# Kernel tuning notes

Measured on AMD Instinct MI355X. Metric: run time of the kernel, lower is better.

The kernel has to match this reference:

```python
import jax, jax.numpy as jnp
import numpy as np

D = 512
B, N = 8, 2048

def setup_inputs() -> dict:
    key = jax.random.key(0)
    ks = jax.random.split(key, 11)
    s = 1.0 / np.sqrt(D)
    return {
        "X": jax.random.normal(ks[0], (B, N, D), dtype=jnp.float32),
        "intensity": jax.random.uniform(ks[1], (B, N, N), dtype=jnp.float32),
        "WQ_w": jax.random.normal(ks[2], (D, D), dtype=jnp.float32) * s,
        "WQ_b": jax.random.normal(ks[3], (D,), dtype=jnp.float32) * 0.01,
        "WK_w": jax.random.normal(ks[4], (D, D), dtype=jnp.float32) * s,
        "WK_b": jax.random.normal(ks[5], (D,), dtype=jnp.float32) * 0.01,
        "WV_w": jax.random.normal(ks[6], (D, D), dtype=jnp.float32) * s,
        "WV_b": jax.random.normal(ks[7], (D,), dtype=jnp.float32) * 0.01,
        "out_w": jax.random.normal(ks[8], (D, D), dtype=jnp.float32) * s,
        "out_b": jax.random.normal(ks[9], (D,), dtype=jnp.float32) * 0.01,
    }

def reference(X, intensity, WQ_w, WQ_b, WK_w, WK_b, WV_w, WV_b, out_w, out_b):
    # torch Linear: y = x @ W.T + b  (W is [out, in])
    q = jnp.einsum('bnd,ed->bne', X, WQ_w) + WQ_b          # [B,N,D]
    k = jnp.einsum('bnd,ed->bne', X, WK_w) + WK_b          # [B,N,D]
    v = jnp.einsum('bnd,ed->bne', X, WV_w) + WV_b          # [B,N,D]
    scale = 1.0 / np.sqrt(D).astype(np.float32)
    scores = jnp.einsum('bqd,bkd->bqk', q, k) * scale      # [B,N,N]
    attn = jax.nn.softmax(scores, axis=-1) + intensity     # post-softmax additive bias
    out = jnp.einsum('bqk,bkd->bqd', attn, v)              # [B,N,D]
    return jnp.einsum('bnd,ed->bne', out, out_w) + out_b
```

## Files before the change

kernel.cpp:

```cpp
#include <hip/hip_runtime.h>
#include <stdint.h>

typedef unsigned short ushort_t;
typedef __attribute__((__ext_vector_type__(8))) __bf16 bf16x8;
typedef __attribute__((__ext_vector_type__(4))) float f32x4;

__device__ inline ushort_t f2bf(float f) {
    unsigned int u = __float_as_uint(f);
    u = u + 0x7FFFu + ((u >> 16) & 1u);
    return (ushort_t)(u >> 16);
}
__device__ inline float bf2f(ushort_t h) {
    return __uint_as_float(((unsigned int)h) << 16);
}

#define GLOAD16(gp, lp) __builtin_amdgcn_global_load_lds( \
    (__attribute__((address_space(1))) void*)(gp),        \
    (__attribute__((address_space(3))) void*)(lp), 16, 0, 0)

template<int MODE, int BN, int BK>
__global__ __launch_bounds__(256)
void gemm_nt(const ushort_t* __restrict__ A, const ushort_t* __restrict__ B,
             void* __restrict__ Cv, const float* __restrict__ bias,
             int K, int lda, int ldb, int ldc, float scale,
             long long sA, long long sB, long long sC)
{
    constexpr int WN  = BN / 2;
    constexpr int NR  = WN / 16;
    constexpr int GPR = BK / 8;
    constexpr int AG  = 128 * GPR;
    constexpr int BG  = BN * GPR;
    __shared__ __align__(16) char lds[(128 + BN) * BK * 2];
    char* ldsA = lds;
    char* ldsB = lds + 128 * BK * 2;

    const int t = threadIdx.x;

    const int gx = gridDim.x, gy = gridDim.y;
    const int nwg = gx * gy * gridDim.z;
    int h = (blockIdx.z * gy + blockIdx.y) * gx + blockIdx.x;
    int logical = (h & 7) * (nwg >> 3) + (h >> 3);
    const int bx = logical % gx;
    const int tmp = logical / gx;
    const int by = tmp % gy;
    const int z  = tmp / gy;

    A += (size_t)z * (size_t)sA;
    B += (size_t)z * (size_t)sB;

    const int rowBase = by * 128;
    const int colBase = bx * BN;

    const int w    = t >> 6;
    const int lane = t & 63;
    const int wr = w >> 1, wc = w & 1;
    const int lr = lane & 15, lg = lane >> 4;

    f32x4 acc[4][NR];
#pragma unroll
    for (int i = 0; i < 4; ++i)
#pragma unroll
        for (int j = 0; j < NR; ++j)
            acc[i][j] = (f32x4){0.f, 0.f, 0.f, 0.f};

    for (int kt = 0; kt < K; kt += BK) {
#pragma unroll
        for (int i = 0; i < AG / 256; ++i) {
            const int L = i * 256 + t;
            const int row = L / GPR, g = L % GPR;
            GLOAD16(A + (size_t)(rowBase + row) * (size_t)lda + (kt + g * 8),
                    ldsA + L * 16);
        }
#pragma unroll
        for (int i = 0; i < BG / 256; ++i) {
            const int L = i * 256 + t;
            const int row = L / GPR, g = L % GPR;
            GLOAD16(B + (size_t)(colBase + row) * (size_t)ldb + (kt + g * 8),
                    ldsB + L * 16);
        }
        __syncthreads();

        const bf16x8* A8 = (const bf16x8*)ldsA;
        const bf16x8* B8 = (const bf16x8*)ldsB;
#pragma unroll
        for (int kk = 0; kk < BK / 32; ++kk) {
            bf16x8 af[4], bq[NR];
#pragma unroll
            for (int mi = 0; mi < 4; ++mi)
                af[mi] = A8[(wr * 64 + mi * 16 + lr) * GPR + kk * 4 + lg];
#pragma unroll
            for (int ni = 0; ni < NR; ++ni)
                bq[ni] = B8[(wc * WN + ni * 16 + lr) * GPR + kk * 4 + lg];
#pragma unroll
            for (int mi = 0; mi < 4; ++mi)
#pragma unroll
                for (int ni = 0; ni < NR; ++ni)
                    acc[mi][ni] = __builtin_amdgcn_mfma_f32_16x16x32_bf16(
                        af[mi], bq[ni], acc[mi][ni], 0, 0, 0);
        }
        __syncthreads();
    }

#pragma unroll
    for (int mi = 0; mi < 4; ++mi) {
#pragma unroll
        for (int ni = 0; ni < NR; ++ni) {
#pragma unroll
            for (int r = 0; r < 4; ++r) {
                const int grow = rowBase + wr * 64 + mi * 16 + lg * 4 + r;
                const int gcol = colBase + wc * WN + ni * 16 + lr;
                float v = acc[mi][ni][r] * scale;
                if (MODE == 0) {
                    if (bias) v += bias[gcol];
                    ushort_t* C = (ushort_t*)Cv + (size_t)z * (size_t)sC;
                    C[(size_t)grow * (size_t)ldc + gcol] = f2bf(v);
                } else if (MODE == 3) {
                    float* C = (float*)Cv;
                    C[(size_t)grow * (size_t)ldc + gcol] = v + bias[gcol];
                } else if (MODE == 4) {
                    v += bias[gcol];
                    const int seg = gcol >> 9, c = gcol & 511;
                    ushort_t* C = (ushort_t*)Cv;
                    C[(size_t)seg * 8388608 + (size_t)grow * 512 + c] = f2bf(v);
                } else {
                    ushort_t* C = (ushort_t*)Cv + (size_t)z * (size_t)sC;
                    C[(size_t)grow * (size_t)ldc + gcol] = f2bf(__expf(v));
                }
            }
        }
    }
}

__global__ __launch_bounds__(256)
void transpose_v(const ushort_t* __restrict__ V, ushort_t* __restrict__ Vt)
{
    __shared__ ushort_t lds[64][68];
    const int t = threadIdx.x;
    const int nBase = blockIdx.x * 64;
    const int dBase = blockIdx.y * 64;
    const size_t b = blockIdx.z;
    const ushort_t* src = V + b * 1048576;
    ushort_t* dst = Vt + b * 1048576;
#pragma unroll
    for (int i = 0; i < 2; ++i) {
        int s = i * 256 + t;
        int n = s >> 3, dg = s & 7;
        union { ushort_t h[8]; uint4 u; } p;
        p.u = *(const uint4*)(src + (size_t)(nBase + n) * 512 + dBase + dg * 8);
#pragma unroll
        for (int j = 0; j < 8; ++j) lds[n][dg * 8 + j] = p.h[j];
    }
    __syncthreads();
#pragma unroll
    for (int i = 0; i < 2; ++i) {
        int s = i * 256 + t;
        int d = s >> 3, ng = s & 7;
        union { ushort_t h[8]; uint4 u; } p;
#pragma unroll
        for (int j = 0; j < 8; ++j) p.h[j] = lds[ng * 8 + j][d];
        *(uint4*)(dst + (size_t)(dBase + d) * 2048 + nBase + ng * 8) = p.u;
    }
}

__global__ __launch_bounds__(256)
void cvt_bf16(const float* __restrict__ src, ushort_t* __restrict__ dst, int n4)
{
    int i = blockIdx.x * 256 + threadIdx.x;
    if (i >= n4) return;
    float4 v = ((const float4*)src)[i];
    union { ushort_t h[4]; uint2 u; } p;
    p.h[0] = f2bf(v.x); p.h[1] = f2bf(v.y); p.h[2] = f2bf(v.z); p.h[3] = f2bf(v.w);
    ((uint2*)dst)[i] = p.u;
}

__global__ __launch_bounds__(256)
void pack_bias(const float* __restrict__ q, const float* __restrict__ k,
               const float* __restrict__ v, float* __restrict__ dst)
{
    int i = blockIdx.x * 256 + threadIdx.x;
    if (i < 512) dst[i] = q[i];
    else if (i < 1024) dst[i] = k[i - 512];
    else if (i < 1536) dst[i] = v[i - 1024];
}

__global__ __launch_bounds__(256)
void norm_add(ushort_t* __restrict__ E, const float* __restrict__ inten)
{
    const int R = blockIdx.x;
    const int t = threadIdx.x;
    const int w = t >> 6, lane = t & 63;
    ushort_t* erow = E + (size_t)R * 2048;
    const float* irow = inten + (size_t)R * 2048;

    union { ushort_t h[8]; uint4 u; } p;
    p.u = *(const uint4*)(erow + t * 8);
    float f[8];
#pragma unroll
    for (int j = 0; j < 8; ++j) f[j] = bf2f(p.h[j]);

    float s = 0.f;
#pragma unroll
    for (int j = 0; j < 8; ++j) s += f[j];
#pragma unroll
    for (int off = 32; off > 0; off >>= 1) s += __shfl_xor(s, off);

    __shared__ float red[4];
    if (lane == 0) red[w] = s;
    __syncthreads();
    const float inv = 1.f / (red[0] + red[1] + red[2] + red[3]);

    float4 i0 = *(const float4*)(irow + t * 8);
    float4 i1 = *(const float4*)(irow + t * 8 + 4);
    float o[8] = { f[0]*inv + i0.x, f[1]*inv + i0.y, f[2]*inv + i0.z, f[3]*inv + i0.w,
                   f[4]*inv + i1.x, f[5]*inv + i1.y, f[6]*inv + i1.z, f[7]*inv + i1.w };
#pragma unroll
    for (int j = 0; j < 8; ++j) p.h[j] = f2bf(o[j]);
    *(uint4*)(erow + t * 8) = p.u;
}

extern "C" void kernel_launch(void* const* d_in, const int* in_sizes, int n_in,
                              void* d_out, int out_size, void* d_ws, size_t ws_size,
                              hipStream_t stream)
{
    const float* X    = (const float*)d_in[0];
    const float* inten= (const float*)d_in[1];
    const float* WQw  = (const float*)d_in[2];
    const float* WQb  = (const float*)d_in[3];
    const float* WKw  = (const float*)d_in[4];
    const float* WKb  = (const float*)d_in[5];
    const float* WVw  = (const float*)d_in[6];
    const float* WVb  = (const float*)d_in[7];
    const float* Wow  = (const float*)d_in[8];
    const float* Wob  = (const float*)d_in[9];
    float* out = (float*)d_out;

    char* ws = (char*)d_ws;
    ushort_t* Xb    = (ushort_t*)(ws + 0);
    ushort_t* Wqkv  = (ushort_t*)(ws + 16777216);
    ushort_t* Wob2  = (ushort_t*)(ws + 18350080);
    float*    biasP = (float*)   (ws + 18874368);
    ushort_t* QKV   = (ushort_t*)(ws + 19922944);
    ushort_t* out1  = (ushort_t*)(ws + 70254592);
    ushort_t* Sbf   = (ushort_t*)(ws + 87031808);
    ushort_t* Qb = QKV;
    ushort_t* Kb = QKV + 8388608;
    ushort_t* Vrm = QKV + 16777216;
    ushort_t* Vt  = Xb;

    const float scale = 0.044194173824159216f;

    cvt_bf16<<<dim3(8192), dim3(256), 0, stream>>>(X,   Xb, 2097152);
    cvt_bf16<<<dim3(256),  dim3(256), 0, stream>>>(WQw, Wqkv,           65536);
    cvt_bf16<<<dim3(256),  dim3(256), 0, stream>>>(WKw, Wqkv + 262144,  65536);
    cvt_bf16<<<dim3(256),  dim3(256), 0, stream>>>(WVw, Wqkv + 524288,  65536);
    cvt_bf16<<<dim3(256),  dim3(256), 0, stream>>>(Wow, Wob2,           65536);
    pack_bias<<<dim3(6),  dim3(256), 0, stream>>>(WQb, WKb, WVb, biasP);

    gemm_nt<4, 128, 32><<<dim3(12, 128, 1), dim3(256), 0, stream>>>(
        Xb, Wqkv, QKV, biasP, 512, 512, 512, 0, 1.f, 0, 0, 0);

    transpose_v<<<dim3(32, 8, 8), dim3(256), 0, stream>>>(Vrm, Vt);

    gemm_nt<5, 128, 32><<<dim3(16, 16, 8), dim3(256), 0, stream>>>(
        Qb, Kb, Sbf, nullptr, 512, 512, 512, 2048, scale,
        2048LL * 512, 2048LL * 512, 2048LL * 2048);

    norm_add<<<dim3(16384), dim3(256), 0, stream>>>(Sbf, inten);

    gemm_nt<0, 64, 32><<<dim3(8, 16, 8), dim3(256), 0, stream>>>(
        Sbf, Vt, out1, nullptr, 2048, 2048, 2048, 512, 1.f,
        2048LL * 2048, 512LL * 2048, 2048LL * 512);

    gemm_nt<3, 64, 32><<<dim3(8, 128, 1), dim3(256), 0, stream>>>(
        out1, Wob2, out, Wob, 512, 512, 512, 512, 1.f, 0, 0, 0);
}
```

Measured before the change: 243.3 us.

## Fuse softmax normalization and intensity add into PV GEMM A-tile load

Removes the separate norm_add pass. The score GEMM epilogue now accumulates per-row exp sums with atomics, a tiny kernel turns them into reciprocals, and the PV GEMM builds each A tile in registers from exp scores, the reciprocal and the fp32 intensity. The standalone X-to-bf16 conversion is also folded into the QKV projection's A load through register staging. The cost is that intensity is now read by every column block of the PV GEMM, leaning on cache for reuse. The A operand also moves from async global-to-LDS loads to register-staged loads with only one-tile prefetch.

```diff
diff --git a/kernel.cpp b/kernel.cpp
--- a/kernel.cpp
+++ b/kernel.cpp
@@ -13,17 +13,22 @@
 __device__ inline float bf2f(ushort_t h) {
     return __uint_as_float(((unsigned int)h) << 16);
 }
+__device__ inline unsigned pack2(float a, float b) {
+    return (unsigned)f2bf(a) | ((unsigned)f2bf(b) << 16);
+}
 
 #define GLOAD16(gp, lp) __builtin_amdgcn_global_load_lds( \
     (__attribute__((address_space(1))) void*)(gp),        \
     (__attribute__((address_space(3))) void*)(lp), 16, 0, 0)
 
-template<int MODE, int BN, int BK>
-__global__ __launch_bounds__(256)
-void gemm_nt(const ushort_t* __restrict__ A, const ushort_t* __restrict__ B,
+template<int MODE, int BN, int BK, int STG>
+__global__ __launch_bounds__(256)
+void gemm_nt(const void* __restrict__ Av, const ushort_t* __restrict__ B,
              void* __restrict__ Cv, const float* __restrict__ bias,
+             const float* __restrict__ If, const float* __restrict__ invp,
              int K, int lda, int ldb, int ldc, float scale,
-             long long sA, long long sB, long long sC)
+             long long sA, long long sB, long long sC,
+             float* __restrict__ rsum)
 {
     constexpr int WN  = BN / 2;
     constexpr int NR  = WN / 16;
@@ -45,7 +50,10 @@
     const int by = tmp % gy;
     const int z  = tmp / gy;
 
-    A += (size_t)z * (size_t)sA;
+    const ushort_t* A = (const ushort_t*)Av + (size_t)z * (size_t)sA;
+    const float* Af   = (const float*)Av + (size_t)z * (size_t)sA;
+    const float* Iz   = If ? If + (size_t)z * (size_t)sA : nullptr;
+    const float* invz = invp ? invp + (size_t)z * 2048 : nullptr;
     B += (size_t)z * (size_t)sB;
 
     const int rowBase = by * 128;
@@ -63,13 +71,67 @@
         for (int j = 0; j < NR; ++j)
             acc[i][j] = (f32x4){0.f, 0.f, 0.f, 0.f};
 
+    float4 xR[4];
+    uint4  eR[2]; float4 iA[2], iB[2];
+    float  invR[2];
+
+    auto loadA = [&](int kt) {
+        if constexpr (STG == 1) {
+#pragma unroll
+            for (int i = 0; i < 2; ++i) {
+                const int L = i * 256 + t, row = L >> 2, g = L & 3;
+                const float* xp = Af + (size_t)(rowBase + row) * (size_t)lda + kt + g * 8;
+                xR[2 * i]     = *(const float4*)xp;
+                xR[2 * i + 1] = *(const float4*)(xp + 4);
+            }
+        } else if constexpr (STG == 2) {
+#pragma unroll
+            for (int i = 0; i < 2; ++i) {
+                const int L = i * 256 + t, row = L >> 2, g = L & 3;
+                const ushort_t* ep = A + (size_t)(rowBase + row) * (size_t)lda + kt + g * 8;
+                eR[i] = *(const uint4*)ep;
+                const float* ip = Iz + (size_t)(rowBase + row) * (size_t)lda + kt + g * 8;
+                iA[i] = *(const float4*)ip;
+                iB[i] = *(const float4*)(ip + 4);
+                invR[i] = invz[rowBase + row];
+            }
+        }
+    };
+    auto storeA = [&]() {
+#pragma unroll
+        for (int i = 0; i < 2; ++i) {
+            const int L = i * 256 + t;
+            uint4 o;
+            if constexpr (STG == 1) {
+                o.x = pack2(xR[2*i].x, xR[2*i].y);
+                o.y = pack2(xR[2*i].z, xR[2*i].w);
+                o.z = pack2(xR[2*i+1].x, xR[2*i+1].y);
+                o.w = pack2(xR[2*i+1].z, xR[2*i+1].w);
+            } else {
+                union { ushort_t hh[8]; uint4 u; } e; e.u = eR[i];
+                const float iv = invR[i];
+                o.x = pack2(bf2f(e.hh[0]) * iv + iA[i].x, bf2f(e.hh[1]) * iv + iA[i].y);
+                o.y = pack2(bf2f(e.hh[2]) * iv + iA[i].z, bf2f(e.hh[3]) * iv + iA[i].w);
+                o.z = pack2(bf2f(e.hh[4]) * iv + iB[i].x, bf2f(e.hh[5]) * iv + iB[i].y);
+                o.w = pack2(bf2f(e.hh[6]) * iv + iB[i].z, bf2f(e.hh[7]) * iv + iB[i].w);
+            }
+            *(uint4*)(ldsA + (size_t)L * 16) = o;
+        }
+    };
+
+    if constexpr (STG != 0) loadA(0);
+
     for (int kt = 0; kt < K; kt += BK) {
-#pragma unroll
-        for (int i = 0; i < AG / 256; ++i) {
-            const int L = i * 256 + t;
-            const int row = L / GPR, g = L % GPR;
-            GLOAD16(A + (size_t)(rowBase + row) * (size_t)lda + (kt + g * 8),
-                    ldsA + L * 16);
+        if constexpr (STG == 0) {
+#pragma unroll
+            for (int i = 0; i < AG / 256; ++i) {
+                const int L = i * 256 + t;
+                const int row = L / GPR, g = L % GPR;
+                GLOAD16(A + (size_t)(rowBase + row) * (size_t)lda + (kt + g * 8),
+                        ldsA + L * 16);
+            }
+        } else {
+            storeA();
         }
 #pragma unroll
         for (int i = 0; i < BG / 256; ++i) {
@@ -78,6 +140,7 @@
             GLOAD16(B + (size_t)(colBase + row) * (size_t)ldb + (kt + g * 8),
                     ldsB + L * 16);
         }
+        if constexpr (STG != 0) { if (kt + BK < K) loadA(kt + BK); }
         __syncthreads();
 
         const bf16x8* A8 = (const bf16x8*)ldsA;
@@ -99,6 +162,14 @@
                         af[mi], bq[ni], acc[mi][ni], 0, 0, 0);
         }
         __syncthreads();
+    }
+
+    float rs[4][4];
+    if (MODE == 5) {
+#pragma unroll
+        for (int mi = 0; mi < 4; ++mi)
+#pragma unroll
+            for (int r = 0; r < 4; ++r) rs[mi][r] = 0.f;
     }
 
 #pragma unroll
@@ -123,8 +194,28 @@
                     ushort_t* C = (ushort_t*)Cv;
                     C[(size_t)seg * 8388608 + (size_t)grow * 512 + c] = f2bf(v);
                 } else {
+                    float e = __expf(v);
                     ushort_t* C = (ushort_t*)Cv + (size_t)z * (size_t)sC;
-                    C[(size_t)grow * (size_t)ldc + gcol] = f2bf(__expf(v));
+                    C[(size_t)grow * (size_t)ldc + gcol] = f2bf(e);
+                    rs[mi][r] += e;
+                }
+            }
+        }
+    }
+
+    if (MODE == 5) {
+#pragma unroll
+        for (int mi = 0; mi < 4; ++mi) {
+#pragma unroll
+            for (int r = 0; r < 4; ++r) {
+                float s = rs[mi][r];
+                s += __shfl_xor(s, 1);
+                s += __shfl_xor(s, 2);
+                s += __shfl_xor(s, 4);
+                s += __shfl_xor(s, 8);
+                if (lr == 0) {
+                    const int grow = rowBase + wr * 64 + mi * 16 + lg * 4 + r;
+                    atomicAdd(&rsum[z * 2048 + grow], s);
                 }
             }
         }
@@ -184,38 +275,17 @@
 }
 
 __global__ __launch_bounds__(256)
-void norm_add(ushort_t* __restrict__ E, const float* __restrict__ inten)
-{
-    const int R = blockIdx.x;
-    const int t = threadIdx.x;
-    const int w = t >> 6, lane = t & 63;
-    ushort_t* erow = E + (size_t)R * 2048;
-    const float* irow = inten + (size_t)R * 2048;
-
-    union { ushort_t h[8]; uint4 u; } p;
-    p.u = *(const uint4*)(erow + t * 8);
-    float f[8];
-#pragma unroll
-    for (int j = 0; j < 8; ++j) f[j] = bf2f(p.h[j]);
-
-    float s = 0.f;
-#pragma unroll
-    for (int j = 0; j < 8; ++j) s += f[j];
-#pragma unroll
-    for (int off = 32; off > 0; off >>= 1) s += __shfl_xor(s, off);
-
-    __shared__ float red[4];
-    if (lane == 0) red[w] = s;
-    __syncthreads();
-    const float inv = 1.f / (red[0] + red[1] + red[2] + red[3]);
-
-    float4 i0 = *(const float4*)(irow + t * 8);
-    float4 i1 = *(const float4*)(irow + t * 8 + 4);
-    float o[8] = { f[0]*inv + i0.x, f[1]*inv + i0.y, f[2]*inv + i0.z, f[3]*inv + i0.w,
-                   f[4]*inv + i1.x, f[5]*inv + i1.y, f[6]*inv + i1.z, f[7]*inv + i1.w };
-#pragma unroll
-    for (int j = 0; j < 8; ++j) p.h[j] = f2bf(o[j]);
-    *(uint4*)(erow + t * 8) = p.u;
+void zero_f32(float* __restrict__ p, int n)
+{
+    int i = blockIdx.x * 256 + threadIdx.x;
+    if (i < n) p[i] = 0.f;
+}
+
+__global__ __launch_bounds__(256)
+void recip_f32(float* __restrict__ p, int n)
+{
+    int i = blockIdx.x * 256 + threadIdx.x;
+    if (i < n) p[i] = 1.0f / p[i];
 }
 
 extern "C" void kernel_launch(void* const* d_in, const int* in_sizes, int n_in,
@@ -235,42 +305,46 @@
     float* out = (float*)d_out;
 
     char* ws = (char*)d_ws;
-    ushort_t* Xb    = (ushort_t*)(ws + 0);
+    ushort_t* Vt    = (ushort_t*)(ws + 0);
     ushort_t* Wqkv  = (ushort_t*)(ws + 16777216);
     ushort_t* Wob2  = (ushort_t*)(ws + 18350080);
     float*    biasP = (float*)   (ws + 18874368);
+    float*    rowsum= (float*)   (ws + 18882560);
     ushort_t* QKV   = (ushort_t*)(ws + 19922944);
     ushort_t* out1  = (ushort_t*)(ws + 70254592);
     ushort_t* Sbf   = (ushort_t*)(ws + 87031808);
-    ushort_t* Qb = QKV;
-    ushort_t* Kb = QKV + 8388608;
+    ushort_t* Qb  = QKV;
+    ushort_t* Kb  = QKV + 8388608;
     ushort_t* Vrm = QKV + 16777216;
-    ushort_t* Vt  = Xb;
 
     const float scale = 0.044194173824159216f;
 
-    cvt_bf16<<<dim3(8192), dim3(256), 0, stream>>>(X,   Xb, 2097152);
-    cvt_bf16<<<dim3(256),  dim3(256), 0, stream>>>(WQw, Wqkv,           65536);
-    cvt_bf16<<<dim3(256),  dim3(256), 0, stream>>>(WKw, Wqkv + 262144,  65536);
-    cvt_bf16<<<dim3(256),  dim3(256), 0, stream>>>(WVw, Wqkv + 524288,  65536);
-    cvt_bf16<<<dim3(256),  dim3(256), 0, stream>>>(Wow, Wob2,           65536);
-    pack_bias<<<dim3(6),  dim3(256), 0, stream>>>(WQb, WKb, WVb, biasP);
-
-    gemm_nt<4, 128, 32><<<dim3(12, 128, 1), dim3(256), 0, stream>>>(
-        Xb, Wqkv, QKV, biasP, 512, 512, 512, 0, 1.f, 0, 0, 0);
+    cvt_bf16<<<dim3(256), dim3(256), 0, stream>>>(WQw, Wqkv,          65536);
+    cvt_bf16<<<dim3(256), dim3(256), 0, stream>>>(WKw, Wqkv + 262144, 65536);
+    cvt_bf16<<<dim3(256), dim3(256), 0, stream>>>(WVw, Wqkv + 524288, 65536);
+    cvt_bf16<<<dim3(256), dim3(256), 0, stream>>>(Wow, Wob2,          65536);
+    pack_bias<<<dim3(6), dim3(256), 0, stream>>>(WQb, WKb, WVb, biasP);
+    zero_f32<<<dim3(64), dim3(256), 0, stream>>>(rowsum, 16384);
+
+    gemm_nt<4, 128, 32, 1><<<dim3(12, 128, 1), dim3(256), 0, stream>>>(
+        X, Wqkv, QKV, biasP, nullptr, nullptr,
+        512, 512, 512, 0, 1.f, 0, 0, 0, nullptr);
 
     transpose_v<<<dim3(32, 8, 8), dim3(256), 0, stream>>>(Vrm, Vt);
 
-    gemm_nt<5, 128, 32><<<dim3(16, 16, 8), dim3(256), 0, stream>>>(
-        Qb, Kb, Sbf, nullptr, 512, 512, 512, 2048, scale,
-        2048LL * 512, 2048LL * 512, 2048LL * 2048);
-
-    norm_add<<<dim3(16384), dim3(256), 0, stream>>>(Sbf, inten);
-
-    gemm_nt<0, 64, 32><<<dim3(8, 16, 8), dim3(256), 0, stream>>>(
-        Sbf, Vt, out1, nullptr, 2048, 2048, 2048, 512, 1.f,
-        2048LL * 2048, 512LL * 2048, 2048LL * 512);
-
-    gemm_nt<3, 64, 32><<<dim3(8, 128, 1), dim3(256), 0, stream>>>(
-        out1, Wob2, out, Wob, 512, 512, 512, 512, 1.f, 0, 0, 0);
-}
+    gemm_nt<5, 128, 32, 0><<<dim3(16, 16, 8), dim3(256), 0, stream>>>(
+        Qb, Kb, Sbf, nullptr, nullptr, nullptr,
+        512, 512, 512, 2048, scale,
+        2048LL * 512, 2048LL * 512, 2048LL * 2048, rowsum);
+
+    recip_f32<<<dim3(64), dim3(256), 0, stream>>>(rowsum, 16384);
+
+    gemm_nt<0, 64, 32, 2><<<dim3(8, 16, 8), dim3(256), 0, stream>>>(
+        Sbf, Vt, out1, nullptr, inten, rowsum,
+        2048, 2048, 2048, 512, 1.f,
+        2048LL * 2048, 512LL * 2048, 2048LL * 512, nullptr);
+
+    gemm_nt<3, 64, 32, 0><<<dim3(8, 128, 1), dim3(256), 0, stream>>>(
+        out1, Wob2, out, Wob, nullptr, nullptr,
+        512, 512, 512, 512, 1.f, 0, 0, 0, nullptr);
+}
```

Result: slower. 319.6 us (+31.4%).

## Fuse softmax row-sum into score GEMM epilogue via atomics; flatten normalize kernel

Applied to the files above, without the earlier changes.

The score GEMM epilogue now accumulates per-row sums of exp values, reduces them across lanes with shuffles, and atomically adds them to a row-sum buffer that is zeroed beforehand. The per-row norm_add kernel, which reread each row to compute its sum, is replaced by a grid-stride elementwise kernel that scales by the precomputed inverse sum and adds intensity. This removes the in-kernel reduction and block sync. The cost is float atomics, an extra zeroing launch, and row sums taken in fp32 before bf16 rounding. The bf16 copy of X also moves to its own workspace region instead of sharing space with the transposed V.

```diff
diff --git a/kernel.cpp b/kernel.cpp
--- a/kernel.cpp
+++ b/kernel.cpp
@@ -23,7 +23,8 @@
 void gemm_nt(const ushort_t* __restrict__ A, const ushort_t* __restrict__ B,
              void* __restrict__ Cv, const float* __restrict__ bias,
              int K, int lda, int ldb, int ldc, float scale,
-             long long sA, long long sB, long long sC)
+             long long sA, long long sB, long long sC,
+             float* __restrict__ rsum)
 {
     constexpr int WN  = BN / 2;
     constexpr int NR  = WN / 16;
@@ -99,6 +100,14 @@
                         af[mi], bq[ni], acc[mi][ni], 0, 0, 0);
         }
         __syncthreads();
+    }
+
+    float rs[4][4];
+    if (MODE == 5) {
+#pragma unroll
+        for (int mi = 0; mi < 4; ++mi)
+#pragma unroll
+            for (int r = 0; r < 4; ++r) rs[mi][r] = 0.f;
     }
 
 #pragma unroll
@@ -123,8 +132,28 @@
                     ushort_t* C = (ushort_t*)Cv;
                     C[(size_t)seg * 8388608 + (size_t)grow * 512 + c] = f2bf(v);
                 } else {
+                    float e = __expf(v);
                     ushort_t* C = (ushort_t*)Cv + (size_t)z * (size_t)sC;
-                    C[(size_t)grow * (size_t)ldc + gcol] = f2bf(__expf(v));
+                    C[(size_t)grow * (size_t)ldc + gcol] = f2bf(e);
+                    rs[mi][r] += e;
+                }
+            }
+        }
+    }
+
+    if (MODE == 5) {
+#pragma unroll
+        for (int mi = 0; mi < 4; ++mi) {
+#pragma unroll
+            for (int r = 0; r < 4; ++r) {
+                float s = rs[mi][r];
+                s += __shfl_xor(s, 1);
+                s += __shfl_xor(s, 2);
+                s += __shfl_xor(s, 4);
+                s += __shfl_xor(s, 8);
+                if (lr == 0) {
+                    const int grow = rowBase + wr * 64 + mi * 16 + lg * 4 + r;
+                    atomicAdd(&rsum[z * 2048 + grow], s);
                 }
             }
         }
@@ -184,38 +213,34 @@
 }
 
 __global__ __launch_bounds__(256)
-void norm_add(ushort_t* __restrict__ E, const float* __restrict__ inten)
-{
-    const int R = blockIdx.x;
-    const int t = threadIdx.x;
-    const int w = t >> 6, lane = t & 63;
-    ushort_t* erow = E + (size_t)R * 2048;
-    const float* irow = inten + (size_t)R * 2048;
-
-    union { ushort_t h[8]; uint4 u; } p;
-    p.u = *(const uint4*)(erow + t * 8);
-    float f[8];
-#pragma unroll
-    for (int j = 0; j < 8; ++j) f[j] = bf2f(p.h[j]);
-
-    float s = 0.f;
-#pragma unroll
-    for (int j = 0; j < 8; ++j) s += f[j];
-#pragma unroll
-    for (int off = 32; off > 0; off >>= 1) s += __shfl_xor(s, off);
-
-    __shared__ float red[4];
-    if (lane == 0) red[w] = s;
-    __syncthreads();
-    const float inv = 1.f / (red[0] + red[1] + red[2] + red[3]);
-
-    float4 i0 = *(const float4*)(irow + t * 8);
-    float4 i1 = *(const float4*)(irow + t * 8 + 4);
-    float o[8] = { f[0]*inv + i0.x, f[1]*inv + i0.y, f[2]*inv + i0.z, f[3]*inv + i0.w,
-                   f[4]*inv + i1.x, f[5]*inv + i1.y, f[6]*inv + i1.z, f[7]*inv + i1.w };
-#pragma unroll
-    for (int j = 0; j < 8; ++j) p.h[j] = f2bf(o[j]);
-    *(uint4*)(erow + t * 8) = p.u;
+void zero_f32(float* __restrict__ p, int n)
+{
+    int i = blockIdx.x * 256 + threadIdx.x;
+    if (i < n) p[i] = 0.f;
+}
+
+__global__ __launch_bounds__(256)
+void norm_flat(ushort_t* __restrict__ E, const float* __restrict__ rowsum,
+               const float* __restrict__ inten)
+{
+    const int nG = 4194304;
+    for (int g = blockIdx.x * 256 + threadIdx.x; g < nG; g += gridDim.x * 256) {
+        const size_t e0 = (size_t)g * 8;
+        const float iv = 1.0f / rowsum[e0 >> 11];
+        union { ushort_t h[8]; uint4 u; } p;
+        p.u = *(const uint4*)(E + e0);
+        float4 i0 = *(const float4*)(inten + e0);
+        float4 i1 = *(const float4*)(inten + e0 + 4);
+        p.h[0] = f2bf(bf2f(p.h[0]) * iv + i0.x);
+        p.h[1] = f2bf(bf2f(p.h[1]) * iv + i0.y);
+        p.h[2] = f2bf(bf2f(p.h[2]) * iv + i0.z);
+        p.h[3] = f2bf(bf2f(p.h[3]) * iv + i0.w);
+        p.h[4] = f2bf(bf2f(p.h[4]) * iv + i1.x);
+        p.h[5] = f2bf(bf2f(p.h[5]) * iv + i1.y);
+        p.h[6] = f2bf(bf2f(p.h[6]) * iv + i1.z);
+        p.h[7] = f2bf(bf2f(p.h[7]) * iv + i1.w);
+        *(uint4*)(E + e0) = p.u;
+    }
 }
 
 extern "C" void kernel_launch(void* const* d_in, const int* in_sizes, int n_in,
@@ -235,42 +260,44 @@
     float* out = (float*)d_out;
 
     char* ws = (char*)d_ws;
-    ushort_t* Xb    = (ushort_t*)(ws + 0);
+    ushort_t* Vt    = (ushort_t*)(ws + 0);
     ushort_t* Wqkv  = (ushort_t*)(ws + 16777216);
     ushort_t* Wob2  = (ushort_t*)(ws + 18350080);
     float*    biasP = (float*)   (ws + 18874368);
+    float*    rowsum= (float*)   (ws + 18882560);
     ushort_t* QKV   = (ushort_t*)(ws + 19922944);
     ushort_t* out1  = (ushort_t*)(ws + 70254592);
     ushort_t* Sbf   = (ushort_t*)(ws + 87031808);
-    ushort_t* Qb = QKV;
-    ushort_t* Kb = QKV + 8388608;
+    ushort_t* Xb    = (ushort_t*)(ws + 154140672);
+    ushort_t* Qb  = QKV;
+    ushort_t* Kb  = QKV + 8388608;
     ushort_t* Vrm = QKV + 16777216;
-    ushort_t* Vt  = Xb;
 
     const float scale = 0.044194173824159216f;
 
     cvt_bf16<<<dim3(8192), dim3(256), 0, stream>>>(X,   Xb, 2097152);
-    cvt_bf16<<<dim3(256),  dim3(256), 0, stream>>>(WQw, Wqkv,           65536);
-    cvt_bf16<<<dim3(256),  dim3(256), 0, stream>>>(WKw, Wqkv + 262144,  65536);
-    cvt_bf16<<<dim3(256),  dim3(256), 0, stream>>>(WVw, Wqkv + 524288,  65536);
-    cvt_bf16<<<dim3(256),  dim3(256), 0, stream>>>(Wow, Wob2,           65536);
-    pack_bias<<<dim3(6),  dim3(256), 0, stream>>>(WQb, WKb, WVb, biasP);
+    cvt_bf16<<<dim3(256),  dim3(256), 0, stream>>>(WQw, Wqkv,          65536);
+    cvt_bf16<<<dim3(256),  dim3(256), 0, stream>>>(WKw, Wqkv + 262144, 65536);
+    cvt_bf16<<<dim3(256),  dim3(256), 0, stream>>>(WVw, Wqkv + 524288, 65536);
+    cvt_bf16<<<dim3(256),  dim3(256), 0, stream>>>(Wow, Wob2,          65536);
+    pack_bias<<<dim3(6), dim3(256), 0, stream>>>(WQb, WKb, WVb, biasP);
+    zero_f32<<<dim3(64), dim3(256), 0, stream>>>(rowsum, 16384);
 
     gemm_nt<4, 128, 32><<<dim3(12, 128, 1), dim3(256), 0, stream>>>(
-        Xb, Wqkv, QKV, biasP, 512, 512, 512, 0, 1.f, 0, 0, 0);
+        Xb, Wqkv, QKV, biasP, 512, 512, 512, 0, 1.f, 0, 0, 0, nullptr);
 
     transpose_v<<<dim3(32, 8, 8), dim3(256), 0, stream>>>(Vrm, Vt);
 
     gemm_nt<5, 128, 32><<<dim3(16, 16, 8), dim3(256), 0, stream>>>(
         Qb, Kb, Sbf, nullptr, 512, 512, 512, 2048, scale,
-        2048LL * 512, 2048LL * 512, 2048LL * 2048);
-
-    norm_add<<<dim3(16384), dim3(256), 0, stream>>>(Sbf, inten);
+        2048LL * 512, 2048LL * 512, 2048LL * 2048, rowsum);
+
+    norm_flat<<<dim3(2048), dim3(256), 0, stream>>>(Sbf, rowsum, inten);
 
     gemm_nt<0, 64, 32><<<dim3(8, 16, 8), dim3(256), 0, stream>>>(
         Sbf, Vt, out1, nullptr, 2048, 2048, 2048, 512, 1.f,
-        2048LL * 2048, 512LL * 2048, 2048LL * 512);
+        2048LL * 2048, 512LL * 2048, 2048LL * 512, nullptr);
 
     gemm_nt<3, 64, 32><<<dim3(8, 128, 1), dim3(256), 0, stream>>>(
-        out1, Wob2, out, Wob, 512, 512, 512, 512, 1.f, 0, 0, 0);
-}
+        out1, Wob2, out, Wob, 512, 512, 512, 512, 1.f, 0, 0, 0, nullptr);
+}
```

New measurement: 265.7 us. 1.09x slower.

## Double-buffer LDS tiles in GEMM to overlap global loads with MFMA

Applied to the files above, without the earlier changes.

Splits the GEMM mainloop into a stage step and an MFMA step and ping-pongs between two LDS buffers, so the next K-tile's global-to-LDS loads are in flight while the current tile is multiplied. This targets load latency that was exposed by the load-sync-compute-sync loop. It doubles LDS use per block, which may lower occupancy. The loop assumes an even K/BK count. Xb is moved to a separate workspace offset so Vt no longer aliases it.

```diff
diff --git a/kernel.cpp b/kernel.cpp
--- a/kernel.cpp
+++ b/kernel.cpp
@@ -30,9 +30,13 @@
     constexpr int GPR = BK / 8;
     constexpr int AG  = 128 * GPR;
     constexpr int BG  = BN * GPR;
-    __shared__ __align__(16) char lds[(128 + BN) * BK * 2];
-    char* ldsA = lds;
-    char* ldsB = lds + 128 * BK * 2;
+    constexpr int ABYTES = 128 * BK * 2;
+    constexpr int BBYTES = BN * BK * 2;
+    __shared__ __align__(16) char lds[2 * (ABYTES + BBYTES)];
+    char* const ldsA0 = lds;
+    char* const ldsB0 = lds + ABYTES;
+    char* const ldsA1 = lds + ABYTES + BBYTES;
+    char* const ldsB1 = lds + 2 * ABYTES + BBYTES;
 
     const int t = threadIdx.x;
 
@@ -63,25 +67,25 @@
         for (int j = 0; j < NR; ++j)
             acc[i][j] = (f32x4){0.f, 0.f, 0.f, 0.f};
 
-    for (int kt = 0; kt < K; kt += BK) {
+    auto stage = [&](int kt, char* dA, char* dB) {
 #pragma unroll
         for (int i = 0; i < AG / 256; ++i) {
             const int L = i * 256 + t;
             const int row = L / GPR, g = L % GPR;
             GLOAD16(A + (size_t)(rowBase + row) * (size_t)lda + (kt + g * 8),
-                    ldsA + L * 16);
+                    dA + L * 16);
         }
 #pragma unroll
         for (int i = 0; i < BG / 256; ++i) {
             const int L = i * 256 + t;
             const int row = L / GPR, g = L % GPR;
             GLOAD16(B + (size_t)(colBase + row) * (size_t)ldb + (kt + g * 8),
-                    ldsB + L * 16);
-        }
-        __syncthreads();
-
-        const bf16x8* A8 = (const bf16x8*)ldsA;
-        const bf16x8* B8 = (const bf16x8*)ldsB;
+                    dB + L * 16);
+        }
+    };
+    auto mfma_phase = [&](const char* la, const char* lb) {
+        const bf16x8* A8 = (const bf16x8*)la;
+        const bf16x8* B8 = (const bf16x8*)lb;
 #pragma unroll
         for (int kk = 0; kk < BK / 32; ++kk) {
             bf16x8 af[4], bq[NR];
@@ -98,6 +102,17 @@
                     acc[mi][ni] = __builtin_amdgcn_mfma_f32_16x16x32_bf16(
                         af[mi], bq[ni], acc[mi][ni], 0, 0, 0);
         }
+    };
+
+    const int NT = K / BK;
+    stage(0, ldsA0, ldsB0);
+    __syncthreads();
+    for (int it = 0; it < NT; it += 2) {
+        stage((it + 1) * BK, ldsA1, ldsB1);
+        mfma_phase(ldsA0, ldsB0);
+        __syncthreads();
+        if (it + 2 < NT) stage((it + 2) * BK, ldsA0, ldsB0);
+        mfma_phase(ldsA1, ldsB1);
         __syncthreads();
     }
 
@@ -235,26 +250,26 @@
     float* out = (float*)d_out;
 
     char* ws = (char*)d_ws;
-    ushort_t* Xb    = (ushort_t*)(ws + 0);
+    ushort_t* Vt    = (ushort_t*)(ws + 0);
     ushort_t* Wqkv  = (ushort_t*)(ws + 16777216);
     ushort_t* Wob2  = (ushort_t*)(ws + 18350080);
     float*    biasP = (float*)   (ws + 18874368);
     ushort_t* QKV   = (ushort_t*)(ws + 19922944);
     ushort_t* out1  = (ushort_t*)(ws + 70254592);
     ushort_t* Sbf   = (ushort_t*)(ws + 87031808);
-    ushort_t* Qb = QKV;
-    ushort_t* Kb = QKV + 8388608;
+    ushort_t* Xb    = (ushort_t*)(ws + 154140672);
+    ushort_t* Qb  = QKV;
+    ushort_t* Kb  = QKV + 8388608;
     ushort_t* Vrm = QKV + 16777216;
-    ushort_t* Vt  = Xb;
 
     const float scale = 0.044194173824159216f;
 
     cvt_bf16<<<dim3(8192), dim3(256), 0, stream>>>(X,   Xb, 2097152);
-    cvt_bf16<<<dim3(256),  dim3(256), 0, stream>>>(WQw, Wqkv,           65536);
-    cvt_bf16<<<dim3(256),  dim3(256), 0, stream>>>(WKw, Wqkv + 262144,  65536);
-    cvt_bf16<<<dim3(256),  dim3(256), 0, stream>>>(WVw, Wqkv + 524288,  65536);
-    cvt_bf16<<<dim3(256),  dim3(256), 0, stream>>>(Wow, Wob2,           65536);
-    pack_bias<<<dim3(6),  dim3(256), 0, stream>>>(WQb, WKb, WVb, biasP);
+    cvt_bf16<<<dim3(256),  dim3(256), 0, stream>>>(WQw, Wqkv,          65536);
+    cvt_bf16<<<dim3(256),  dim3(256), 0, stream>>>(WKw, Wqkv + 262144, 65536);
+    cvt_bf16<<<dim3(256),  dim3(256), 0, stream>>>(WVw, Wqkv + 524288, 65536);
+    cvt_bf16<<<dim3(256),  dim3(256), 0, stream>>>(Wow, Wob2,          65536);
+    pack_bias<<<dim3(6), dim3(256), 0, stream>>>(WQb, WKb, WVb, biasP);
 
     gemm_nt<4, 128, 32><<<dim3(12, 128, 1), dim3(256), 0, stream>>>(
         Xb, Wqkv, QKV, biasP, 512, 512, 512, 0, 1.f, 0, 0, 0);
```

New measurement: 242.1 us. No clear change (-0.5%).
